# Optimization experiments

Measured on AMD Instinct MI355X. Metric: run time of the kernel, lower is better.

The kernel has to match this reference:

```python
import jax, jax.numpy as jnp
import numpy as np

NUM_CLASSES = 3
POS_T, NEG_T = 0.5, 0.3
RATIO = 3
W_OBJ, W_CLS, W_LOC = 1.0, 1.0, 2.0


def _pairwise_iou(a, b):
    # a: [N,4] anchors, b: [G,4] gt boxes, xyxy
    ix1 = jnp.maximum(a[:, None, 0], b[None, :, 0])
    iy1 = jnp.maximum(a[:, None, 1], b[None, :, 1])
    ix2 = jnp.minimum(a[:, None, 2], b[None, :, 2])
    iy2 = jnp.minimum(a[:, None, 3], b[None, :, 3])
    inter = jnp.clip(ix2 - ix1, 0) * jnp.clip(iy2 - iy1, 0)
    area_a = (a[:, 2] - a[:, 0]) * (a[:, 3] - a[:, 1])
    area_b = (b[:, 2] - b[:, 0]) * (b[:, 3] - b[:, 1])
    union = area_a[:, None] + area_b[None, :] - inter
    return inter / jnp.maximum(union, 1e-9)


def _masked_mean(x, m):
    c = m.sum()
    return jnp.where(c > 0, (x * m).sum() / jnp.maximum(c, 1.0), 0.0)


def _per_image(pred, anc, ax, ay, aw, ah, boxes_gt, labels_gt):
    # pred: [N, 5+nc]; anc: [N,4]; boxes_gt: [G,4]; labels_gt: [G] in 1..nc
    iou = _pairwise_iou(anc, boxes_gt)              # [N, G]
    best = jnp.argmax(iou, axis=1)
    best_iou = jnp.max(iou, axis=1)
    pos = best_iou >= POS_T
    neg = best_iou < NEG_T
    mb = boxes_gt[best]                             # matched boxes [N,4]
    ml = labels_gt[best]                            # matched labels [N]
    obj_logit = pred[:, 4]
    cls_logit = pred[:, 5:]
    obj_t = pos.astype(pred.dtype)
    # BCEWithLogits (numerically stable)
    obj_loss = jnp.maximum(obj_logit, 0) - obj_logit * obj_t + jnp.log1p(jnp.exp(-jnp.abs(obj_logit)))
    # hard negative mining: top-(3*num_pos) detached obj losses among negatives
    num_pos = pos.sum()
    k = jnp.minimum(RATIO * num_pos, neg.sum())
    cand = jnp.where(neg, jax.lax.stop_gradient(obj_loss), -1.0)
    order = jnp.argsort(-cand)
    ranks = jnp.zeros_like(order).at[order].set(jnp.arange(order.shape[0], dtype=order.dtype))
    sel_neg = neg & (ranks < k)
    loss_obj = _masked_mean(obj_loss, (pos | sel_neg).astype(pred.dtype))
    # classification over positives, labels shifted to 0-based
    logp = jax.nn.log_softmax(cls_logit, axis=-1)
    tgt = jnp.clip(ml - 1, 0)
    ce = -jnp.take_along_axis(logp, tgt[:, None], axis=1)[:, 0]
    loss_cls = _masked_mean(ce, pos.astype(pred.dtype))
    # localization over positives: SmoothL1 on encoded offsets
    gx = (mb[:, 0] + mb[:, 2]) * 0.5
    gy = (mb[:, 1] + mb[:, 3]) * 0.5
    gw = jnp.maximum(mb[:, 2] - mb[:, 0], 1e-6)
    gh = jnp.maximum(mb[:, 3] - mb[:, 1], 1e-6)
    loc_tgt = jnp.stack([(gx - ax) / aw, (gy - ay) / ah,
                         jnp.log(gw / aw), jnp.log(gh / ah)], axis=1)
    d = pred[:, :4] - loc_tgt
    ad = jnp.abs(d)
    sl1 = jnp.where(ad < 1.0, 0.5 * d * d, ad - 0.5)  # [N,4]
    pm = pos.astype(pred.dtype)
    cnt = 4.0 * pm.sum()
    loss_loc = jnp.where(cnt > 0, (sl1 * pm[:, None]).sum() / jnp.maximum(cnt, 1.0), 0.0)
    return loss_obj, loss_cls, loss_loc


def _detection_loss(preds, ancs, gt_boxes, gt_labels):
    B = preds[0].shape[0]
    obj_s = 0.0
    cls_s = 0.0
    loc_s = 0.0
    for pred, anc in zip(preds, ancs):
        Bp, C, H, W = pred.shape
        p = jnp.transpose(pred, (0, 2, 3, 1)).reshape(Bp, -1, 5 + NUM_CLASSES)
        ax = (anc[:, 0] + anc[:, 2]) * 0.5
        ay = (anc[:, 1] + anc[:, 3]) * 0.5
        aw = jnp.maximum(anc[:, 2] - anc[:, 0], 1e-6)
        ah = jnp.maximum(anc[:, 3] - anc[:, 1], 1e-6)
        lo, lc, ll = jax.vmap(
            lambda pb, bb, lb: _per_image(pb, anc, ax, ay, aw, ah, bb, lb)
        )(p, gt_boxes, gt_labels)
        obj_s = obj_s + lo.sum()
        cls_s = cls_s + lc.sum()
        loc_s = loc_s + ll.sum()
    obj_m = obj_s / B
    cls_m = cls_s / B
    loc_m = loc_s / B
    total = W_OBJ * obj_m + W_CLS * cls_m + W_LOC * loc_m
    return total, obj_m, cls_m, loc_m


def setup_inputs() -> dict:
    key = jax.random.key(0)
    k = jax.random.split(key, 8)
    B, G, A = 32, 50, 3
    img = 512.0
    scales = [(128, 128), (64, 64), (32, 32)]
    C = A * (5 + NUM_CLASSES)  # 24

    def make_anchors(H, W):
        stride = img / H
        ys, xs = np.meshgrid(np.arange(H), np.arange(W), indexing="ij")
        cx = (xs + 0.5) * stride
        cy = (ys + 0.5) * stride
        per = []
        for s in (1.0, 1.5, 2.0):
            half = s * stride
            per.append(np.stack([cx - half, cy - half, cx + half, cy + half], axis=-1).reshape(-1, 4))
        b = np.stack(per, axis=1).reshape(-1, 4)  # [H*W*A, 4], A innermost
        return jnp.asarray(b, dtype=jnp.float32)

    preds = [jax.random.normal(k[i], (B, C, H, W), dtype=jnp.float32) for i, (H, W) in enumerate(scales)]
    ancs = [make_anchors(H, W) for (H, W) in scales]
    cx = jax.random.uniform(k[3], (B, G)) * 384.0 + 64.0
    cy = jax.random.uniform(k[4], (B, G)) * 384.0 + 64.0
    w = jax.random.uniform(k[5], (B, G)) * 112.0 + 16.0
    h = jax.random.uniform(k[6], (B, G)) * 112.0 + 16.0
    gt_boxes = jnp.stack([cx - w / 2, cy - h / 2, cx + w / 2, cy + h / 2], axis=-1).astype(jnp.float32)
    gt_labels = jax.random.randint(k[7], (B, G), 1, NUM_CLASSES + 1)
    return {"p0": preds[0], "p1": preds[1], "p2": preds[2],
            "a0": ancs[0], "a1": ancs[1], "a2": ancs[2],
            "gt_boxes": gt_boxes, "gt_labels": gt_labels}


def reference(p0, p1, p2, a0, a1, a2, gt_boxes, gt_labels):
    return _detection_loss([p0, p1, p2], [a0, a1, a2], gt_boxes, gt_labels)
```

## Files before the change

### kernel.cpp

```cpp
#include <hip/hip_runtime.h>

#define WS_ACC_POS   0
#define WS_ACC_NEG   96
#define WS_ACC_OBJ   192
#define WS_ACC_CLS   288
#define WS_ACC_LOC   384
#define WS_SENT      480
#define WS_H1        512
#define WS_TOTAL_U32 (512 + 96*2048*2)

#define SUM_SCALE    33554432.0f
#define INV_SUM_SCALE (1.0f/33554432.0f)

__device__ __forceinline__ float sl1f(float d){
  float ad = fabsf(d); return ad < 1.f ? 0.5f*d*d : ad - 0.5f;
}
__device__ __forceinline__ unsigned int rec_cnt(unsigned int v){
  return (v >= 0xA0000000u) ? (v - 0xAAAAAAAAu) : v;
}

__global__ __launch_bounds__(256) void k_main(
    const float* __restrict__ p0, const float* __restrict__ p1, const float* __restrict__ p2,
    const float* __restrict__ gtb, const int* __restrict__ gtl,
    unsigned int* __restrict__ ws)
{
  const int id = blockIdx.x;
  int s, bIm, chunk, H, lw; const float* p;
  if (id < 2048){ s=0; H=128; lw=7; chunk=id>>5;            bIm=id&31;          p=p0; }
  else if (id < 2560){ s=1; H=64; lw=6; chunk=(id-2048)>>5; bIm=(id-2048)&31;   p=p1; }
  else {              s=2; H=32; lw=5; chunk=(id-2560)>>5;  bIm=(id-2560)&31;   p=p2; }
  const int W = H, HW = H*W;
  const float stride = 512.0f/(float)H;
  const int g = s*32 + bIm;
  const int tid = threadIdx.x;

  __shared__ float4 sBox[52];
  __shared__ float  sArea[52], sGx[52], sGy[52], sGw[52], sGh[52];
  __shared__ int    sLbl[52];
  __shared__ int    sNk;
  __shared__ unsigned long long sH[2048];
  __shared__ float  sRF[3][4];
  __shared__ unsigned int sRU[2][4];

  if (tid < 64){
    const int ymin = (chunk*256)>>lw;
    const int rowc = 256>>lw;
    const float by1 = ((float)ymin+0.5f)*stride - 2.0f*stride;
    const float by2 = ((float)(ymin+rowc-1)+0.5f)*stride + 2.0f*stride;
    bool keep=false; float4 gb=make_float4(0,0,0,0); int lbl=0;
    if (tid < 50){
      gb  = *(const float4*)(gtb + ((size_t)bIm*50 + tid)*4);
      lbl = gtl[bIm*50 + tid];
      keep = (fminf(by2, gb.w) - fmaxf(by1, gb.y)) > 0.f;
    }
    unsigned long long m = __ballot(keep);
    if (keep){
      int idx = __popcll(m & ((1ull<<tid)-1ull));
      sBox[idx]=gb;
      sArea[idx]=(gb.z-gb.x)*(gb.w-gb.y);
      sGx[idx]=(gb.x+gb.z)*0.5f;  sGy[idx]=(gb.y+gb.w)*0.5f;
      sGw[idx]=fmaxf(gb.z-gb.x,1e-6f); sGh[idx]=fmaxf(gb.w-gb.y,1e-6f);
      sLbl[idx]=lbl;
    }
    if (tid==0) sNk = __popcll(m);
  }
  for (int h=tid; h<2048; h+=256) sH[h]=0ull;
  __syncthreads();

  const int nk = sNk;
  const int hw  = chunk*256 + tid;
  const int hwW = chunk*256 + (tid & ~63);
  const int y = hw>>lw, x = hw&(W-1);
  const float cx = ((float)x+0.5f)*stride, cy = ((float)y+0.5f)*stride;

  const float* pb = p + (size_t)bIm*24*HW + hw;
  float xo[3];
  #pragma unroll
  for (int a=0;a<3;a++) xo[a] = pb[(size_t)(a*8+4)*HW];

  const int wxlo = (W >= 64) ? (hwW & (W-1)) : 0;
  const int wxhi = (W >= 64) ? (wxlo + 63)   : (W-1);
  const int wylo = hwW>>lw, wyhi = (hwW+63)>>lw;
  const float m2 = 2.0f*stride;
  const float wx1 = ((float)wxlo+0.5f)*stride - m2;
  const float wx2 = ((float)wxhi+0.5f)*stride + m2;
  const float wy1 = ((float)wylo+0.5f)*stride - m2;
  const float wy2 = ((float)wyhi+0.5f)*stride + m2;

  float half[3]; half[0]=stride; half[1]=1.5f*stride; half[2]=2.0f*stride;
  float areaA[3], bi[3], bu[3]; int bj[3];
  #pragma unroll
  for (int a=0;a<3;a++){
    const float aw = 2.0f*half[a];
    areaA[a]=aw*aw; bi[a]=0.f; bu[a]=1e-9f; bj[a]=0;
  }
  for (int j=0;j<nk;j++){
    const float4 gb = sBox[j];
    if (gb.x >= wx2 || gb.z <= wx1 || gb.y >= wy2 || gb.w <= wy1) continue;
    const float ar = sArea[j];
    #pragma unroll
    for (int a=0;a<3;a++){
      const float iy1 = fmaxf(cy-half[a], gb.y), iy2 = fminf(cy+half[a], gb.w);
      const float ih  = fmaxf(iy2-iy1, 0.f);
      const float ix1 = fmaxf(cx-half[a], gb.x), ix2 = fminf(cx+half[a], gb.z);
      const float iw  = fmaxf(ix2-ix1, 0.f);
      const float inter = iw*ih;
      const float un = areaA[a] + ar - inter;
      if (inter*bu[a] > bi[a]*un){ bi[a]=inter; bu[a]=un; bj[a]=j; }
    }
  }

  int accPos=0, accNeg=0;
  float accObj=0.f, accCls=0.f, accLoc=0.f;
  #pragma unroll
  for (int a=0;a<3;a++){
    const float bestIou = bi[a]/bu[a];
    const bool pos = bestIou >= 0.5f;
    const bool neg = bestIou < 0.3f;
    float objl = fmaxf(xo[a],0.f) - (pos ? xo[a] : 0.f)
               + __logf(1.f + __expf(-fabsf(xo[a])));
    objl = fmaxf(objl, 0.f);
    if (neg){
      accNeg++;
      const unsigned int bin = min(__float_as_uint(objl)>>20, 2047u);
      const unsigned long long pack =
          (1ull<<48) | (unsigned long long)__float2uint_rn(objl * SUM_SCALE);
      atomicAdd(&sH[bin], pack);
    }
    if (pos){
      accPos++; accObj += objl;
      const int jb = bj[a];
      const float aw = 2.0f*half[a];
      const float c0=pb[(size_t)(a*8+5)*HW], c1=pb[(size_t)(a*8+6)*HW], c2=pb[(size_t)(a*8+7)*HW];
      const float mm = fmaxf(fmaxf(c0,c1),c2);
      const float lse = mm + __logf(__expf(c0-mm)+__expf(c1-mm)+__expf(c2-mm));
      const int t = max(sLbl[jb]-1, 0);
      const float ct = (t==0)?c0 : (t==1)?c1 : c2;
      accCls += lse - ct;
      const float tx = (sGx[jb]-cx)/aw;
      const float ty = (sGy[jb]-cy)/aw;
      const float tw = __logf(sGw[jb]/aw);
      const float th = __logf(sGh[jb]/aw);
      accLoc += sl1f(pb[(size_t)(a*8+0)*HW]-tx) + sl1f(pb[(size_t)(a*8+1)*HW]-ty)
              + sl1f(pb[(size_t)(a*8+2)*HW]-tw) + sl1f(pb[(size_t)(a*8+3)*HW]-th);
    }
  }

  #pragma unroll
  for (int o=32;o;o>>=1){
    accPos += __shfl_down(accPos,o,64);
    accNeg += __shfl_down(accNeg,o,64);
    accObj += __shfl_down(accObj,o,64);
    accCls += __shfl_down(accCls,o,64);
    accLoc += __shfl_down(accLoc,o,64);
  }
  if ((tid & 63)==0){
    const int w = tid>>6;
    sRU[0][w]=(unsigned)accPos; sRU[1][w]=(unsigned)accNeg;
    sRF[0][w]=accObj; sRF[1][w]=accCls; sRF[2][w]=accLoc;
  }
  __syncthreads();
  if (tid==0){
    float* wf = (float*)ws;
    unsigned pc=0, nc=0; float ob=0,cl=0,lc=0;
    #pragma unroll
    for (int w=0;w<4;w++){ pc+=sRU[0][w]; nc+=sRU[1][w]; ob+=sRF[0][w]; cl+=sRF[1][w]; lc+=sRF[2][w]; }
    if (pc) atomicAdd(&ws[WS_ACC_POS+g], pc);
    if (nc) atomicAdd(&ws[WS_ACC_NEG+g], nc);
    if (ob!=0.f) atomicAdd(&wf[WS_ACC_OBJ+g], ob);
    if (cl!=0.f) atomicAdd(&wf[WS_ACC_CLS+g], cl);
    if (lc!=0.f) atomicAdd(&wf[WS_ACC_LOC+g], lc);
  }
  unsigned long long* gH = (unsigned long long*)(ws + WS_H1) + (size_t)g*2048;
  for (int h=tid; h<2048; h+=256){
    const unsigned long long v = sH[h];
    if (v) atomicAdd(&gH[h], v);
  }
}

__device__ __forceinline__ void wave_suffix_find(
    const unsigned int* __restrict__ binsLDS, const unsigned int* __restrict__ scC,
    unsigned int target, int* sTie, int* sR, int lane)
{
  const unsigned int c4 = scC[4*lane]+scC[4*lane+1]+scC[4*lane+2]+scC[4*lane+3];
  unsigned int incl = c4;
  #pragma unroll
  for (int off=1; off<64; off<<=1){
    unsigned int yv = __shfl_down(incl, off, 64);
    if (lane+off < 64) incl += yv;
  }
  const unsigned int excl = incl - c4;
  if (excl < target && incl >= target){
    unsigned int cum = excl; int fs = 4*lane;
    for (int ss=3; ss>=0; ss--){
      unsigned int c = scC[4*lane+ss];
      if (cum + c >= target){ fs = 4*lane+ss; break; }
      cum += c;
    }
    for (int bin=fs*8+7; bin>=fs*8; bin--){
      unsigned int c = binsLDS[bin];
      if (cum + c >= target){ *sTie = bin; *sR = (int)(target - cum); break; }
      cum += c;
    }
  }
}

__global__ __launch_bounds__(256) void k_select(unsigned int* __restrict__ ws,
                                                float* __restrict__ out){
  const int g = blockIdx.x, tid = threadIdx.x;
  float* wf = (float*)ws;
  __shared__ unsigned int hc[2048];
  __shared__ float        hs[2048];
  __shared__ unsigned int scC[256];
  __shared__ int sTie1, sR1;
  __shared__ float sRed[4];

  const int pos  = (int)rec_cnt(ws[WS_ACC_POS+g]);
  const int negc = (int)rec_cnt(ws[WS_ACC_NEG+g]);
  const int k = min(3*pos, negc);
  float selSum = 0.f;

  if (k > 0){
    const unsigned long long base =
        (ws[WS_SENT]==0xAAAAAAAAu) ? 0xAAAAAAAAAAAAAAAAull : 0ull;
    const unsigned long long* gH =
        (const unsigned long long*)(ws + WS_H1) + (size_t)g*2048;
    #pragma unroll
    for (int i=0;i<8;i++){
      const unsigned long long d = gH[tid+256*i] - base;
      hc[tid+256*i] = (unsigned int)(d>>48);
      hs[tid+256*i] = (float)(d & 0xFFFFFFFFFFFFull) * INV_SUM_SCALE;
    }
    __syncthreads();
    unsigned int sum=0;
    #pragma unroll
    for (int i=0;i<8;i++) sum += hc[tid*8+i];
    scC[tid]=sum;
    __syncthreads();
    if (tid < 64) wave_suffix_find(hc, scC, (unsigned)k, &sTie1, &sR1, tid);
    __syncthreads();
    const int tie1 = sTie1;
    float above = 0.f;
    #pragma unroll
    for (int i=0;i<8;i++){
      const int bin = tid*8+i;
      if (bin > tie1) above += hs[bin];
    }
    #pragma unroll
    for (int o=32;o;o>>=1) above += __shfl_down(above,o,64);
    if ((tid&63)==0) sRed[tid>>6] = above;
    __syncthreads();
    if (tid==0){
      const float ab = sRed[0]+sRed[1]+sRed[2]+sRed[3];
      selSum = ab + (float)sR1 * (hs[tie1]/(float)hc[tie1]);
    }
  }
  if (tid==0){
    const int cObj = pos + k;
    const float lo = (cObj>0) ? (wf[WS_ACC_OBJ+g]+selSum)/(float)cObj : 0.f;
    const float lc = (pos>0)  ? wf[WS_ACC_CLS+g]/(float)pos           : 0.f;
    const float ll = (pos>0)  ? wf[WS_ACC_LOC+g]/(float)(4*pos)       : 0.f;
    const float invB = 1.f/32.f;
    atomicAdd(out+0, (lo + lc + 2.f*ll)*invB);
    atomicAdd(out+1, lo*invB);
    atomicAdd(out+2, lc*invB);
    atomicAdd(out+3, ll*invB);
  }
}

extern "C" void kernel_launch(void* const* d_in, const int* in_sizes, int n_in,
                              void* d_out, int out_size, void* d_ws, size_t ws_size,
                              hipStream_t stream){
  if (ws_size < (size_t)WS_TOTAL_U32*4) return;
  const float* p0  = (const float*)d_in[0];
  const float* p1  = (const float*)d_in[1];
  const float* p2  = (const float*)d_in[2];
  const float* gtb = (const float*)d_in[6];
  const int*   gtl = (const int*)d_in[7];
  unsigned int* ws = (unsigned int*)d_ws;
  float* out = (float*)d_out;

  hipLaunchKernelGGL(k_main,   dim3(2688), dim3(256), 0, stream, p0,p1,p2,gtb,gtl,ws);
  hipLaunchKernelGGL(k_select, dim3(96),   dim3(256), 0, stream, ws, out);
}
```

Measured before the change: 123.7 us.

## Shrink negative-loss histogram to 192 offset bins and use single-wave select kernel

Cuts the per-group loss histogram from 2048 bins to 192 by subtracting a fixed exponent-bin offset and clamping at both ends. This shrinks the LDS zeroing and the global atomic flush in the main kernel, and the workspace the select kernel reads. The select kernel becomes one 64-thread wave with three bins per lane, doing the prefix scan with shuffles instead of multi-stage LDS passes. It also skips the objective-loss math for anchors that are neither positive nor negative. Clamping values outside the bin range can merge distinct losses into the edge bins and make the top-k sum less exact.

```diff
diff --git a/kernel.cpp b/kernel.cpp
--- a/kernel.cpp
+++ b/kernel.cpp
@@ -7,8 +7,10 @@
 #define WS_ACC_LOC   384
 #define WS_SENT      480
 #define WS_H1        512
-#define WS_TOTAL_U32 (512 + 96*2048*2)
-
+#define WS_TOTAL_U32 (512 + 96*192*2)
+
+#define NBINS        192
+#define BIN_OFF      872
 #define SUM_SCALE    33554432.0f
 #define INV_SUM_SCALE (1.0f/33554432.0f)
 
@@ -38,7 +40,7 @@
   __shared__ float  sArea[52], sGx[52], sGy[52], sGw[52], sGh[52];
   __shared__ int    sLbl[52];
   __shared__ int    sNk;
-  __shared__ unsigned long long sH[2048];
+  __shared__ unsigned long long sH[NBINS];
   __shared__ float  sRF[3][4];
   __shared__ unsigned int sRU[2][4];
 
@@ -64,7 +66,7 @@
     }
     if (tid==0) sNk = __popcll(m);
   }
-  for (int h=tid; h<2048; h+=256) sH[h]=0ull;
+  if (tid < NBINS) sH[tid]=0ull;
   __syncthreads();
 
   const int nk = sNk;
@@ -117,32 +119,33 @@
     const float bestIou = bi[a]/bu[a];
     const bool pos = bestIou >= 0.5f;
     const bool neg = bestIou < 0.3f;
-    float objl = fmaxf(xo[a],0.f) - (pos ? xo[a] : 0.f)
-               + __logf(1.f + __expf(-fabsf(xo[a])));
-    objl = fmaxf(objl, 0.f);
-    if (neg){
-      accNeg++;
-      const unsigned int bin = min(__float_as_uint(objl)>>20, 2047u);
-      const unsigned long long pack =
-          (1ull<<48) | (unsigned long long)__float2uint_rn(objl * SUM_SCALE);
-      atomicAdd(&sH[bin], pack);
-    }
-    if (pos){
-      accPos++; accObj += objl;
-      const int jb = bj[a];
-      const float aw = 2.0f*half[a];
-      const float c0=pb[(size_t)(a*8+5)*HW], c1=pb[(size_t)(a*8+6)*HW], c2=pb[(size_t)(a*8+7)*HW];
-      const float mm = fmaxf(fmaxf(c0,c1),c2);
-      const float lse = mm + __logf(__expf(c0-mm)+__expf(c1-mm)+__expf(c2-mm));
-      const int t = max(sLbl[jb]-1, 0);
-      const float ct = (t==0)?c0 : (t==1)?c1 : c2;
-      accCls += lse - ct;
-      const float tx = (sGx[jb]-cx)/aw;
-      const float ty = (sGy[jb]-cy)/aw;
-      const float tw = __logf(sGw[jb]/aw);
-      const float th = __logf(sGh[jb]/aw);
-      accLoc += sl1f(pb[(size_t)(a*8+0)*HW]-tx) + sl1f(pb[(size_t)(a*8+1)*HW]-ty)
-              + sl1f(pb[(size_t)(a*8+2)*HW]-tw) + sl1f(pb[(size_t)(a*8+3)*HW]-th);
+    if (pos || neg){
+      float objl = fmaxf(xo[a],0.f) - (pos ? xo[a] : 0.f)
+                 + __logf(1.f + __expf(-fabsf(xo[a])));
+      objl = fmaxf(objl, 0.f);
+      if (neg){
+        accNeg++;
+        const int bin = min(max((int)(__float_as_uint(objl)>>20) - BIN_OFF, 0), NBINS-1);
+        const unsigned long long pack =
+            (1ull<<48) | (unsigned long long)__float2uint_rn(objl * SUM_SCALE);
+        atomicAdd(&sH[bin], pack);
+      } else {
+        accPos++; accObj += objl;
+        const int jb = bj[a];
+        const float aw = 2.0f*half[a];
+        const float c0=pb[(size_t)(a*8+5)*HW], c1=pb[(size_t)(a*8+6)*HW], c2=pb[(size_t)(a*8+7)*HW];
+        const float mm = fmaxf(fmaxf(c0,c1),c2);
+        const float lse = mm + __logf(__expf(c0-mm)+__expf(c1-mm)+__expf(c2-mm));
+        const int t = max(sLbl[jb]-1, 0);
+        const float ct = (t==0)?c0 : (t==1)?c1 : c2;
+        accCls += lse - ct;
+        const float tx = (sGx[jb]-cx)/aw;
+        const float ty = (sGy[jb]-cy)/aw;
+        const float tw = __logf(sGw[jb]/aw);
+        const float th = __logf(sGh[jb]/aw);
+        accLoc += sl1f(pb[(size_t)(a*8+0)*HW]-tx) + sl1f(pb[(size_t)(a*8+1)*HW]-ty)
+                + sl1f(pb[(size_t)(a*8+2)*HW]-tw) + sl1f(pb[(size_t)(a*8+3)*HW]-th);
+      }
     }
   }
 
@@ -171,49 +174,21 @@
     if (cl!=0.f) atomicAdd(&wf[WS_ACC_CLS+g], cl);
     if (lc!=0.f) atomicAdd(&wf[WS_ACC_LOC+g], lc);
   }
-  unsigned long long* gH = (unsigned long long*)(ws + WS_H1) + (size_t)g*2048;
-  for (int h=tid; h<2048; h+=256){
-    const unsigned long long v = sH[h];
-    if (v) atomicAdd(&gH[h], v);
-  }
-}
-
-__device__ __forceinline__ void wave_suffix_find(
-    const unsigned int* __restrict__ binsLDS, const unsigned int* __restrict__ scC,
-    unsigned int target, int* sTie, int* sR, int lane)
-{
-  const unsigned int c4 = scC[4*lane]+scC[4*lane+1]+scC[4*lane+2]+scC[4*lane+3];
-  unsigned int incl = c4;
-  #pragma unroll
-  for (int off=1; off<64; off<<=1){
-    unsigned int yv = __shfl_down(incl, off, 64);
-    if (lane+off < 64) incl += yv;
-  }
-  const unsigned int excl = incl - c4;
-  if (excl < target && incl >= target){
-    unsigned int cum = excl; int fs = 4*lane;
-    for (int ss=3; ss>=0; ss--){
-      unsigned int c = scC[4*lane+ss];
-      if (cum + c >= target){ fs = 4*lane+ss; break; }
-      cum += c;
-    }
-    for (int bin=fs*8+7; bin>=fs*8; bin--){
-      unsigned int c = binsLDS[bin];
-      if (cum + c >= target){ *sTie = bin; *sR = (int)(target - cum); break; }
-      cum += c;
-    }
-  }
-}
-
-__global__ __launch_bounds__(256) void k_select(unsigned int* __restrict__ ws,
-                                                float* __restrict__ out){
-  const int g = blockIdx.x, tid = threadIdx.x;
+  if (tid < NBINS){
+    const unsigned long long v = sH[tid];
+    if (v){
+      unsigned long long* gH = (unsigned long long*)(ws + WS_H1) + (size_t)g*NBINS;
+      atomicAdd(&gH[tid], v);
+    }
+  }
+}
+
+__global__ __launch_bounds__(64) void k_select(unsigned int* __restrict__ ws,
+                                               float* __restrict__ out){
+  const int g = blockIdx.x, lane = threadIdx.x;
   float* wf = (float*)ws;
-  __shared__ unsigned int hc[2048];
-  __shared__ float        hs[2048];
-  __shared__ unsigned int scC[256];
-  __shared__ int sTie1, sR1;
-  __shared__ float sRed[4];
+  __shared__ int   sTie, sR;
+  __shared__ float sTieAvg;
 
   const int pos  = (int)rec_cnt(ws[WS_ACC_POS+g]);
   const int negc = (int)rec_cnt(ws[WS_ACC_NEG+g]);
@@ -224,38 +199,46 @@
     const unsigned long long base =
         (ws[WS_SENT]==0xAAAAAAAAu) ? 0xAAAAAAAAAAAAAAAAull : 0ull;
     const unsigned long long* gH =
-        (const unsigned long long*)(ws + WS_H1) + (size_t)g*2048;
-    #pragma unroll
-    for (int i=0;i<8;i++){
-      const unsigned long long d = gH[tid+256*i] - base;
-      hc[tid+256*i] = (unsigned int)(d>>48);
-      hs[tid+256*i] = (float)(d & 0xFFFFFFFFFFFFull) * INV_SUM_SCALE;
+        (const unsigned long long*)(ws + WS_H1) + (size_t)g*NBINS;
+    unsigned int c[3]; float sm[3];
+    #pragma unroll
+    for (int j=0;j<3;j++){
+      const unsigned long long d = gH[lane*3+j] - base;
+      c[j]  = (unsigned int)(d>>48);
+      sm[j] = (float)(d & 0xFFFFFFFFFFFFull) * INV_SUM_SCALE;
+    }
+    const unsigned int c3 = c[0]+c[1]+c[2];
+    unsigned int incl = c3;
+    #pragma unroll
+    for (int off=1; off<64; off<<=1){
+      unsigned int yv = __shfl_down(incl, off, 64);
+      if (lane+off < 64) incl += yv;
+    }
+    const unsigned int excl = incl - c3;
+    if (lane==0){ sTie = -1; sR = 0; sTieAvg = 0.f; }
+    if (excl < (unsigned)k && incl >= (unsigned)k){
+      unsigned int cum = excl;
+      #pragma unroll
+      for (int j=2;j>=0;j--){
+        const unsigned int cc = c[j];
+        if (cum + cc >= (unsigned)k){
+          sTie = lane*3+j; sR = (int)((unsigned)k - cum);
+          sTieAvg = sm[j]/(float)cc;
+          break;
+        }
+        cum += cc;
+      }
     }
     __syncthreads();
-    unsigned int sum=0;
-    #pragma unroll
-    for (int i=0;i<8;i++) sum += hc[tid*8+i];
-    scC[tid]=sum;
-    __syncthreads();
-    if (tid < 64) wave_suffix_find(hc, scC, (unsigned)k, &sTie1, &sR1, tid);
-    __syncthreads();
-    const int tie1 = sTie1;
+    const int tie = sTie;
     float above = 0.f;
     #pragma unroll
-    for (int i=0;i<8;i++){
-      const int bin = tid*8+i;
-      if (bin > tie1) above += hs[bin];
-    }
+    for (int j=0;j<3;j++) if (lane*3+j > tie) above += sm[j];
     #pragma unroll
     for (int o=32;o;o>>=1) above += __shfl_down(above,o,64);
-    if ((tid&63)==0) sRed[tid>>6] = above;
-    __syncthreads();
-    if (tid==0){
-      const float ab = sRed[0]+sRed[1]+sRed[2]+sRed[3];
-      selSum = ab + (float)sR1 * (hs[tie1]/(float)hc[tie1]);
-    }
-  }
-  if (tid==0){
+    selSum = above + (float)sR * sTieAvg;
+  }
+  if (lane==0){
     const int cObj = pos + k;
     const float lo = (cObj>0) ? (wf[WS_ACC_OBJ+g]+selSum)/(float)cObj : 0.f;
     const float lc = (pos>0)  ? wf[WS_ACC_CLS+g]/(float)pos           : 0.f;
@@ -281,5 +264,5 @@
   float* out = (float*)d_out;
 
   hipLaunchKernelGGL(k_main,   dim3(2688), dim3(256), 0, stream, p0,p1,p2,gtb,gtl,ws);
-  hipLaunchKernelGGL(k_select, dim3(96),   dim3(256), 0, stream, ws, out);
-}
+  hipLaunchKernelGGL(k_select, dim3(96),   dim3(64),  0, stream, ws, out);
+}
```

Result: no change. 122.6 us (-0.9%).
